# Kernel tuning notes

Measured on AMD Instinct MI355X. Metric: run time of the kernel, lower is better.

## Reference

```python
import jax, jax.numpy as jnp
import numpy as np

TOP_K = 4
EPS = 1e-6


def setup_inputs() -> dict:
    key = jax.random.key(0)
    k1, k2, k3 = jax.random.split(key, 3)
    B, Q, N, H, W = 4, 200, 32, 256, 256
    pred_masks = jax.random.normal(k1, (B, Q, H, W), dtype=jnp.float32)
    pred_logits = jax.random.normal(k2, (B, Q, 2), dtype=jnp.float32)
    gt_masks = (jax.random.uniform(k3, (B, N, H, W)) < 0.3).astype(jnp.float32)
    return {"pred_masks": pred_masks, "pred_logits": pred_logits, "gt_masks": gt_masks}


def _combined_scores(pred_masks, pred_logits, gt_masks):
    """IoU * class-score, shape [B, Q, N]."""
    pm = jax.nn.sigmoid(pred_masks)                    # [B,Q,H,W]
    cls = jax.nn.softmax(pred_logits, axis=-1)[..., 1]  # [B,Q]
    B, Q = pm.shape[:2]
    N = gt_masks.shape[1]
    pmf = pm.reshape(B, Q, -1)                         # [B,Q,D]
    tmf = gt_masks.reshape(B, N, -1)                   # [B,N,D]
    inter = jnp.einsum('bqd,bnd->bqn', pmf, tmf)
    union = pmf.sum(-1)[:, :, None] + tmf.sum(-1)[:, None, :] - inter
    iou = inter / (union + EPS)
    return iou * cls[:, :, None]


def _greedy_assign(combined):
    """Greedy per-GT top-k with dedup. combined: [Q,N] -> sel indices [N,k], -1 = dropped."""
    Q = combined.shape[0]
    k = min(TOP_K, Q)

    def step(assigned, col):
        _, idx = jax.lax.top_k(col, k)          # [k] query indices for this GT
        taken = assigned[idx]                   # already assigned -> drop
        sel = jnp.where(taken, -1, idx)
        assigned = assigned.at[idx].set(True)
        return assigned, sel

    _, sels = jax.lax.scan(step, jnp.zeros(Q, dtype=bool), combined.T)
    return sels  # [N, k]


def reference(pred_masks, pred_logits, gt_masks):
    combined = _combined_scores(pred_masks, pred_logits, gt_masks)  # [B,Q,N]
    sels = jax.vmap(_greedy_assign)(combined)                       # [B,N,k]
    B, N, k = sels.shape
    src_idx = sels
    tgt_idx = jnp.broadcast_to(jnp.arange(N, dtype=jnp.int32)[None, :, None], sels.shape)
    valid = sels >= 0
    tgt_idx = jnp.where(valid, tgt_idx, -1)
    return src_idx, tgt_idx, valid
```

## Files before the change

### kernel.cpp

```cpp
#include <hip/hip_runtime.h>
#include <math.h>
#include <stdint.h>

#define BB    4
#define QQ    200
#define NGT   32
#define DD    65536
#define TOPK  4
#define EPSF  1e-6f
#define QP    208

#define QT16  13
#define KG    32
#define KSPAN (DD / KG)
#define KQ    (KSPAN / 4)
#define NIT   (KQ / 32)

typedef float  f32x4  __attribute__((ext_vector_type(4)));
typedef __bf16 bf16x8 __attribute__((ext_vector_type(8)));

#define PERM_HI16 0x07060302u
#define PERM_LO16 0x05040100u

__global__ __launch_bounds__(256) void k_pack(const float* __restrict__ gt,
                                              uint32_t* __restrict__ packed,
                                              float* __restrict__ zero_base) {
    int zidx = blockIdx.x * 256 + threadIdx.x;
    if (zidx < BB * NGT * QP + BB * QP) zero_base[zidx] = 0.0f;

    int blk = blockIdx.x;
    int b = blk >> 6;
    int d0 = ((blk & 63) * 256 + threadIdx.x) * 4;
    uint32_t px = 0, py = 0, pz = 0, pw = 0;
    const float* gb = gt + (size_t)b * NGT * DD + d0;
#pragma unroll
    for (int n = 0; n < NGT; ++n) {
        float4 g = *(const float4*)(gb + (size_t)n * DD);
        px |= (g.x > 0.5f ? 1u : 0u) << n;
        py |= (g.y > 0.5f ? 1u : 0u) << n;
        pz |= (g.z > 0.5f ? 1u : 0u) << n;
        pw |= (g.w > 0.5f ? 1u : 0u) << n;
    }
    *(uint4*)(packed + (size_t)b * DD + d0) = make_uint4(px, py, pz, pw);
}

__global__ __launch_bounds__(256) void k_tsum(const uint32_t* __restrict__ packed,
                                              float* __restrict__ tsum) {
    int b = blockIdx.x >> 5;
    int n = blockIdx.x & 31;
    const uint4* pp = (const uint4*)(packed + (size_t)b * DD);
    int cnt = 0;
    for (int i = threadIdx.x; i < DD / 4; i += 256) {
        uint4 w = pp[i];
        cnt += (int)((w.x >> n) & 1u) + (int)((w.y >> n) & 1u) +
               (int)((w.z >> n) & 1u) + (int)((w.w >> n) & 1u);
    }
#pragma unroll
    for (int off = 32; off; off >>= 1) cnt += __shfl_xor(cnt, off);
    __shared__ int red[4];
    if ((threadIdx.x & 63) == 0) red[threadIdx.x >> 6] = cnt;
    __syncthreads();
    if (threadIdx.x == 0)
        tsum[blockIdx.x] = (float)(red[0] + red[1] + red[2] + red[3]);
}

__global__ __launch_bounds__(256) void k_mfma(const float* __restrict__ pm,
                                              const uint32_t* __restrict__ packed,
                                              float* __restrict__ inter,
                                              float* __restrict__ psum) {
    int blk = blockIdx.x;
    int b   = blk / (QT16 * KG);
    int rem = blk % (QT16 * KG);
    int qt  = rem / KG;
    int kg  = rem % KG;
    int tid = threadIdx.x, lane = tid & 63, wave = tid >> 6;
    int m = lane & 15, quad = lane >> 4;

    int qg_m = qt * 16 + m;
    int qrow = qg_m < QQ ? qg_m : QQ - 1;

    const float*    ap = pm + ((size_t)b * QQ + qrow) * DD
                            + (size_t)kg * KSPAN + wave * KQ + quad * 8;
    const uint32_t* bp = packed + (size_t)b * DD
                                + (size_t)kg * KSPAN + wave * KQ + quad * 8;

    f32x4 cH0 = {0.f,0.f,0.f,0.f}, cL0 = {0.f,0.f,0.f,0.f};
    f32x4 cH1 = {0.f,0.f,0.f,0.f}, cL1 = {0.f,0.f,0.f,0.f};
    float ps = 0.f;

#pragma unroll 2
    for (int it = 0; it < NIT; ++it) {
        float4 a0 = *(const float4*)(ap + it * 32);
        float4 a1 = *(const float4*)(ap + it * 32 + 4);
        uint4  w0 = *(const uint4*)(bp + it * 32);
        uint4  w1 = *(const uint4*)(bp + it * 32 + 4);

        float xs[8] = {a0.x, a0.y, a0.z, a0.w, a1.x, a1.y, a1.z, a1.w};
        uint32_t hu[8], mu[8], lu[8];
#pragma unroll
        for (int i = 0; i < 8; ++i) {
            float x  = xs[i];
            float sg = __builtin_amdgcn_rcpf(1.0f + __expf(-x));
            ps += sg;
            uint32_t u0 = __float_as_uint(sg);
            float hi = __uint_as_float(u0 & 0xFFFF0000u);
            float r1 = sg - hi;
            uint32_t u1 = __float_as_uint(r1);
            float mi = __uint_as_float(u1 & 0xFFFF0000u);
            float r2 = r1 - mi;
            hu[i] = u0; mu[i] = u1; lu[i] = __float_as_uint(r2);
        }
        union { uint4 u; bf16x8 v; } ah, am, al;
        ah.u = make_uint4(__builtin_amdgcn_perm(hu[1], hu[0], PERM_HI16),
                          __builtin_amdgcn_perm(hu[3], hu[2], PERM_HI16),
                          __builtin_amdgcn_perm(hu[5], hu[4], PERM_HI16),
                          __builtin_amdgcn_perm(hu[7], hu[6], PERM_HI16));
        am.u = make_uint4(__builtin_amdgcn_perm(mu[1], mu[0], PERM_HI16),
                          __builtin_amdgcn_perm(mu[3], mu[2], PERM_HI16),
                          __builtin_amdgcn_perm(mu[5], mu[4], PERM_HI16),
                          __builtin_amdgcn_perm(mu[7], mu[6], PERM_HI16));
        al.u = make_uint4(__builtin_amdgcn_perm(lu[1], lu[0], PERM_HI16),
                          __builtin_amdgcn_perm(lu[3], lu[2], PERM_HI16),
                          __builtin_amdgcn_perm(lu[5], lu[4], PERM_HI16),
                          __builtin_amdgcn_perm(lu[7], lu[6], PERM_HI16));

        uint32_t wj[8] = {w0.x, w0.y, w0.z, w0.w, w1.x, w1.y, w1.z, w1.w};
        uint32_t ob[8];
#pragma unroll
        for (int j = 0; j < 8; ++j) {
            uint32_t t = wj[j] >> m;
            ob[j] = (t & 0x10001u) * 0x3F80u;
        }
        union { uint4 u; bf16x8 v; } b0, b1;
        b0.u = make_uint4(__builtin_amdgcn_perm(ob[1], ob[0], PERM_LO16),
                          __builtin_amdgcn_perm(ob[3], ob[2], PERM_LO16),
                          __builtin_amdgcn_perm(ob[5], ob[4], PERM_LO16),
                          __builtin_amdgcn_perm(ob[7], ob[6], PERM_LO16));
        b1.u = make_uint4(__builtin_amdgcn_perm(ob[1], ob[0], PERM_HI16),
                          __builtin_amdgcn_perm(ob[3], ob[2], PERM_HI16),
                          __builtin_amdgcn_perm(ob[5], ob[4], PERM_HI16),
                          __builtin_amdgcn_perm(ob[7], ob[6], PERM_HI16));

        cH0 = __builtin_amdgcn_mfma_f32_16x16x32_bf16(ah.v, b0.v, cH0, 0, 0, 0);
        cL0 = __builtin_amdgcn_mfma_f32_16x16x32_bf16(am.v, b0.v, cL0, 0, 0, 0);
        cL0 = __builtin_amdgcn_mfma_f32_16x16x32_bf16(al.v, b0.v, cL0, 0, 0, 0);
        cH1 = __builtin_amdgcn_mfma_f32_16x16x32_bf16(ah.v, b1.v, cH1, 0, 0, 0);
        cL1 = __builtin_amdgcn_mfma_f32_16x16x32_bf16(am.v, b1.v, cL1, 0, 0, 0);
        cL1 = __builtin_amdgcn_mfma_f32_16x16x32_bf16(al.v, b1.v, cL1, 0, 0, 0);
    }

    ps += __shfl_xor(ps, 16);
    ps += __shfl_xor(ps, 32);
    if (lane < 16) {
        int qg = qt * 16 + m;
        if (qg < QQ) atomicAdd(&psum[b * QP + qg], ps);
    }

    __shared__ float cred[3 * 64 * 9];
    float c8[8];
#pragma unroll
    for (int r = 0; r < 4; ++r) {
        c8[r]     = cH0[r] + cL0[r];
        c8[4 + r] = cH1[r] + cL1[r];
    }
    __syncthreads();
    if (wave > 0) {
        float* dst = cred + ((wave - 1) * 64 + lane) * 9;
#pragma unroll
        for (int r = 0; r < 8; ++r) dst[r] = c8[r];
    }
    __syncthreads();
    if (wave == 0) {
#pragma unroll
        for (int wv = 0; wv < 3; ++wv) {
            const float* sp = cred + (wv * 64 + lane) * 9;
#pragma unroll
            for (int r = 0; r < 8; ++r) c8[r] += sp[r];
        }
#pragma unroll
        for (int r = 0; r < 4; ++r) {
            int qg = qt * 16 + quad * 4 + r;
            if (qg < QQ) {
                atomicAdd(&inter[(b * NGT + m) * QP + qg],      c8[r]);
                atomicAdd(&inter[(b * NGT + 16 + m) * QP + qg], c8[4 + r]);
            }
        }
    }
}

__global__ __launch_bounds__(256) void k_match(const float* __restrict__ inter,
                                               const float* __restrict__ psum,
                                               const float* __restrict__ tsum,
                                               const float* __restrict__ logits,
                                               int* __restrict__ out) {
    int b = blockIdx.x;
    int tid = threadIdx.x, lane = tid & 63, wave = tid >> 6;
    __shared__ int sidx[NGT][TOPK];

    for (int nn = 0; nn < 8; ++nn) {
        int n  = wave * 8 + nn;
        int bn = b * NGT + n;
        float tsn = tsum[bn];
        float v[4];
#pragma unroll
        for (int s = 0; s < 4; ++s) {
            int q = lane + 64 * s;
            if (q < QQ) {
                float iv = inter[(size_t)bn * QP + q];
                float un = psum[b * QP + q] + tsn - iv;
                float l0 = logits[(b * QQ + q) * 2];
                float l1 = logits[(b * QQ + q) * 2 + 1];
                float cl = 1.0f / (1.0f + expf(l0 - l1));
                v[s] = iv / (un + EPSF) * cl;
            } else {
                v[s] = -INFINITY;
            }
        }
        for (int k = 0; k < TOPK; ++k) {
            float bv = -INFINITY;
            int   bi = 0x7fffffff;
#pragma unroll
            for (int s = 0; s < 4; ++s)
                if (v[s] > bv) { bv = v[s]; bi = lane + 64 * s; }
#pragma unroll
            for (int off = 32; off; off >>= 1) {
                float ov = __shfl_xor(bv, off);
                int   oi = __shfl_xor(bi, off);
                if (ov > bv || (ov == bv && oi < bi)) { bv = ov; bi = oi; }
            }
            if (lane == (bi & 63)) v[bi >> 6] = -INFINITY;
            if (lane == 0) sidx[n][k] = bi;
        }
    }
    __syncthreads();

    if (wave == 0) {
        int* src = out;
        int* tgt = out + BB * NGT * TOPK;
        int* val = out + 2 * BB * NGT * TOPK;
        int asg = 0;
        for (int n = 0; n < NGT; ++n) {
            int ids[4] = {sidx[n][0], sidx[n][1], sidx[n][2], sidx[n][3]};
            int newasg = asg;
#pragma unroll
            for (int k = 0; k < TOPK; ++k) {
                int idx = ids[k];
                int owner = idx & 63, slot = idx >> 6;
                int oasg = __shfl(asg, owner);
                int taken = (oasg >> slot) & 1;
                if (lane == owner) newasg |= (1 << slot);
                if (lane == 0) {
                    int o = (b * NGT + n) * TOPK + k;
                    src[o] = taken ? -1 : idx;
                    tgt[o] = taken ? -1 : n;
                    val[o] = taken ? 0 : 1;
                }
            }
            asg = newasg;
        }
    }
}

extern "C" void kernel_launch(void* const* d_in, const int* in_sizes, int n_in,
                              void* d_out, int out_size, void* d_ws, size_t ws_size,
                              hipStream_t stream) {
    const float* pred_masks  = (const float*)d_in[0];
    const float* pred_logits = (const float*)d_in[1];
    const float* gt_masks    = (const float*)d_in[2];

    uint8_t* ws = (uint8_t*)d_ws;
    uint32_t* packed = (uint32_t*)ws;
    float* tsum  = (float*)(ws + (size_t)BB * DD * 4);
    float* inter = tsum + BB * NGT;
    float* psum  = inter + BB * NGT * QP;

    k_pack <<<BB * (DD / 1024), 256, 0, stream>>>(gt_masks, packed, inter);
    k_tsum <<<BB * NGT,         256, 0, stream>>>(packed, tsum);
    k_mfma <<<BB * QT16 * KG,   256, 0, stream>>>(pred_masks, packed, inter, psum);
    k_match<<<BB,               256, 0, stream>>>(inter, psum, tsum, pred_logits, (int*)d_out);
}
```

Before: 364.7 us.

## Stage pred-mask tiles through LDS with double-buffered async global_load_lds

The MFMA kernel now loads the 16-row pred_masks tile into a double-buffered LDS array using global_load_lds with XOR swizzling, prefetching the next 256-wide chunk while computing the current one. Each wave reads its fragment from LDS instead of issuing strided per-lane global loads, and the reduction scratch reuses the same LDS buffer. The aim is coalesced, overlapped loading of the dominant 200×65536 float stream. In exchange it adds a full vmcnt drain and a barrier per chunk, plus 32KB of LDS per block, which may lower occupancy.

```diff
diff --git a/kernel.cpp b/kernel.cpp
--- a/kernel.cpp
+++ b/kernel.cpp
@@ -13,14 +13,22 @@
 #define QT16  13
 #define KG    32
 #define KSPAN (DD / KG)
-#define KQ    (KSPAN / 4)
-#define NIT   (KQ / 32)
+#define BK    256
+#define NCH   (KSPAN / BK)
 
 typedef float  f32x4  __attribute__((ext_vector_type(4)));
 typedef __bf16 bf16x8 __attribute__((ext_vector_type(8)));
 
 #define PERM_HI16 0x07060302u
 #define PERM_LO16 0x05040100u
+
+#define RAW_BARRIER() asm volatile("s_barrier" ::: "memory")
+#define VM_DRAIN()    asm volatile("s_waitcnt vmcnt(0)" ::: "memory")
+
+#define GLOAD_LDS16(gptr, lptr)                                                  \
+    __builtin_amdgcn_global_load_lds(                                            \
+        (const __attribute__((address_space(1))) uint32_t*)(gptr),               \
+        (__attribute__((address_space(3))) uint32_t*)(lptr), 16, 0, 0)
 
 __global__ __launch_bounds__(256) void k_pack(const float* __restrict__ gt,
                                               uint32_t* __restrict__ packed,
@@ -76,77 +84,110 @@
     int tid = threadIdx.x, lane = tid & 63, wave = tid >> 6;
     int m = lane & 15, quad = lane >> 4;
 
-    int qg_m = qt * 16 + m;
-    int qrow = qg_m < QQ ? qg_m : QQ - 1;
-
-    const float*    ap = pm + ((size_t)b * QQ + qrow) * DD
-                            + (size_t)kg * KSPAN + wave * KQ + quad * 8;
-    const uint32_t* bp = packed + (size_t)b * DD
-                                + (size_t)kg * KSPAN + wave * KQ + quad * 8;
+    __shared__ float sA[2][16][BK];
+
+    const float*    pmb = pm + (size_t)b * QQ * DD + (size_t)kg * KSPAN;
+    const uint32_t* pkb = packed + (size_t)b * DD + (size_t)kg * KSPAN;
+
+    int row0 = wave * 4;
+    int qrow[4];
+#pragma unroll
+    for (int i = 0; i < 4; ++i) {
+        int qg = qt * 16 + row0 + i;
+        qrow[i] = qg < QQ ? qg : QQ - 1;
+    }
 
     f32x4 cH0 = {0.f,0.f,0.f,0.f}, cL0 = {0.f,0.f,0.f,0.f};
     f32x4 cH1 = {0.f,0.f,0.f,0.f}, cL1 = {0.f,0.f,0.f,0.f};
     float ps = 0.f;
 
-#pragma unroll 2
-    for (int it = 0; it < NIT; ++it) {
-        float4 a0 = *(const float4*)(ap + it * 32);
-        float4 a1 = *(const float4*)(ap + it * 32 + 4);
-        uint4  w0 = *(const uint4*)(bp + it * 32);
-        uint4  w1 = *(const uint4*)(bp + it * 32 + 4);
-
-        float xs[8] = {a0.x, a0.y, a0.z, a0.w, a1.x, a1.y, a1.z, a1.w};
-        uint32_t hu[8], mu[8], lu[8];
-#pragma unroll
-        for (int i = 0; i < 8; ++i) {
-            float x  = xs[i];
-            float sg = __builtin_amdgcn_rcpf(1.0f + __expf(-x));
-            ps += sg;
-            uint32_t u0 = __float_as_uint(sg);
-            float hi = __uint_as_float(u0 & 0xFFFF0000u);
-            float r1 = sg - hi;
-            uint32_t u1 = __float_as_uint(r1);
-            float mi = __uint_as_float(u1 & 0xFFFF0000u);
-            float r2 = r1 - mi;
-            hu[i] = u0; mu[i] = u1; lu[i] = __float_as_uint(r2);
-        }
-        union { uint4 u; bf16x8 v; } ah, am, al;
-        ah.u = make_uint4(__builtin_amdgcn_perm(hu[1], hu[0], PERM_HI16),
-                          __builtin_amdgcn_perm(hu[3], hu[2], PERM_HI16),
-                          __builtin_amdgcn_perm(hu[5], hu[4], PERM_HI16),
-                          __builtin_amdgcn_perm(hu[7], hu[6], PERM_HI16));
-        am.u = make_uint4(__builtin_amdgcn_perm(mu[1], mu[0], PERM_HI16),
-                          __builtin_amdgcn_perm(mu[3], mu[2], PERM_HI16),
-                          __builtin_amdgcn_perm(mu[5], mu[4], PERM_HI16),
-                          __builtin_amdgcn_perm(mu[7], mu[6], PERM_HI16));
-        al.u = make_uint4(__builtin_amdgcn_perm(lu[1], lu[0], PERM_HI16),
-                          __builtin_amdgcn_perm(lu[3], lu[2], PERM_HI16),
-                          __builtin_amdgcn_perm(lu[5], lu[4], PERM_HI16),
-                          __builtin_amdgcn_perm(lu[7], lu[6], PERM_HI16));
-
-        uint32_t wj[8] = {w0.x, w0.y, w0.z, w0.w, w1.x, w1.y, w1.z, w1.w};
-        uint32_t ob[8];
-#pragma unroll
-        for (int j = 0; j < 8; ++j) {
-            uint32_t t = wj[j] >> m;
-            ob[j] = (t & 0x10001u) * 0x3F80u;
-        }
-        union { uint4 u; bf16x8 v; } b0, b1;
-        b0.u = make_uint4(__builtin_amdgcn_perm(ob[1], ob[0], PERM_LO16),
-                          __builtin_amdgcn_perm(ob[3], ob[2], PERM_LO16),
-                          __builtin_amdgcn_perm(ob[5], ob[4], PERM_LO16),
-                          __builtin_amdgcn_perm(ob[7], ob[6], PERM_LO16));
-        b1.u = make_uint4(__builtin_amdgcn_perm(ob[1], ob[0], PERM_HI16),
-                          __builtin_amdgcn_perm(ob[3], ob[2], PERM_HI16),
-                          __builtin_amdgcn_perm(ob[5], ob[4], PERM_HI16),
-                          __builtin_amdgcn_perm(ob[7], ob[6], PERM_HI16));
-
-        cH0 = __builtin_amdgcn_mfma_f32_16x16x32_bf16(ah.v, b0.v, cH0, 0, 0, 0);
-        cL0 = __builtin_amdgcn_mfma_f32_16x16x32_bf16(am.v, b0.v, cL0, 0, 0, 0);
-        cL0 = __builtin_amdgcn_mfma_f32_16x16x32_bf16(al.v, b0.v, cL0, 0, 0, 0);
-        cH1 = __builtin_amdgcn_mfma_f32_16x16x32_bf16(ah.v, b1.v, cH1, 0, 0, 0);
-        cL1 = __builtin_amdgcn_mfma_f32_16x16x32_bf16(am.v, b1.v, cL1, 0, 0, 0);
-        cL1 = __builtin_amdgcn_mfma_f32_16x16x32_bf16(al.v, b1.v, cL1, 0, 0, 0);
+#pragma unroll
+    for (int i = 0; i < 4; ++i) {
+        int r = row0 + i;
+        const float* gsrc = pmb + (size_t)qrow[i] * DD + ((lane ^ (r & 7)) << 2);
+        GLOAD_LDS16(gsrc, &sA[0][r][0]);
+    }
+    VM_DRAIN();
+    RAW_BARRIER();
+
+    for (int c = 0; c < NCH; ++c) {
+        int buf = c & 1;
+        if (c + 1 < NCH) {
+#pragma unroll
+            for (int i = 0; i < 4; ++i) {
+                int r = row0 + i;
+                const float* gsrc = pmb + (size_t)qrow[i] * DD
+                                        + (size_t)(c + 1) * BK + ((lane ^ (r & 7)) << 2);
+                GLOAD_LDS16(gsrc, &sA[buf ^ 1][r][0]);
+            }
+        }
+
+#pragma unroll
+        for (int st = 0; st < 2; ++st) {
+            int k0 = wave * 64 + st * 32 + quad * 8;
+            int c0 = k0 >> 2;
+            float4 a0 = *(const float4*)&sA[buf][m][(c0 ^ (m & 7)) << 2];
+            float4 a1 = *(const float4*)&sA[buf][m][((c0 + 1) ^ (m & 7)) << 2];
+            const uint32_t* bpc = pkb + (size_t)c * BK + k0;
+            uint4 w0 = *(const uint4*)(bpc);
+            uint4 w1 = *(const uint4*)(bpc + 4);
+
+            float xs[8] = {a0.x, a0.y, a0.z, a0.w, a1.x, a1.y, a1.z, a1.w};
+            uint32_t hu[8], mu[8], lu[8];
+#pragma unroll
+            for (int i = 0; i < 8; ++i) {
+                float x  = xs[i];
+                float sg = __builtin_amdgcn_rcpf(1.0f + __expf(-x));
+                ps += sg;
+                uint32_t u0 = __float_as_uint(sg);
+                float hi = __uint_as_float(u0 & 0xFFFF0000u);
+                float r1 = sg - hi;
+                uint32_t u1 = __float_as_uint(r1);
+                float mi = __uint_as_float(u1 & 0xFFFF0000u);
+                float r2 = r1 - mi;
+                hu[i] = u0; mu[i] = u1; lu[i] = __float_as_uint(r2);
+            }
+            union { uint4 u; bf16x8 v; } ah, am, al;
+            ah.u = make_uint4(__builtin_amdgcn_perm(hu[1], hu[0], PERM_HI16),
+                              __builtin_amdgcn_perm(hu[3], hu[2], PERM_HI16),
+                              __builtin_amdgcn_perm(hu[5], hu[4], PERM_HI16),
+                              __builtin_amdgcn_perm(hu[7], hu[6], PERM_HI16));
+            am.u = make_uint4(__builtin_amdgcn_perm(mu[1], mu[0], PERM_HI16),
+                              __builtin_amdgcn_perm(mu[3], mu[2], PERM_HI16),
+                              __builtin_amdgcn_perm(mu[5], mu[4], PERM_HI16),
+                              __builtin_amdgcn_perm(mu[7], mu[6], PERM_HI16));
+            al.u = make_uint4(__builtin_amdgcn_perm(lu[1], lu[0], PERM_HI16),
+                              __builtin_amdgcn_perm(lu[3], lu[2], PERM_HI16),
+                              __builtin_amdgcn_perm(lu[5], lu[4], PERM_HI16),
+                              __builtin_amdgcn_perm(lu[7], lu[6], PERM_HI16));
+
+            uint32_t wj[8] = {w0.x, w0.y, w0.z, w0.w, w1.x, w1.y, w1.z, w1.w};
+            uint32_t ob[8];
+#pragma unroll
+            for (int j = 0; j < 8; ++j) {
+                uint32_t t = wj[j] >> m;
+                ob[j] = (t & 0x10001u) * 0x3F80u;
+            }
+            union { uint4 u; bf16x8 v; } b0, b1;
+            b0.u = make_uint4(__builtin_amdgcn_perm(ob[1], ob[0], PERM_LO16),
+                              __builtin_amdgcn_perm(ob[3], ob[2], PERM_LO16),
+                              __builtin_amdgcn_perm(ob[5], ob[4], PERM_LO16),
+                              __builtin_amdgcn_perm(ob[7], ob[6], PERM_LO16));
+            b1.u = make_uint4(__builtin_amdgcn_perm(ob[1], ob[0], PERM_HI16),
+                              __builtin_amdgcn_perm(ob[3], ob[2], PERM_HI16),
+                              __builtin_amdgcn_perm(ob[5], ob[4], PERM_HI16),
+                              __builtin_amdgcn_perm(ob[7], ob[6], PERM_HI16));
+
+            cH0 = __builtin_amdgcn_mfma_f32_16x16x32_bf16(ah.v, b0.v, cH0, 0, 0, 0);
+            cL0 = __builtin_amdgcn_mfma_f32_16x16x32_bf16(am.v, b0.v, cL0, 0, 0, 0);
+            cL0 = __builtin_amdgcn_mfma_f32_16x16x32_bf16(al.v, b0.v, cL0, 0, 0, 0);
+            cH1 = __builtin_amdgcn_mfma_f32_16x16x32_bf16(ah.v, b1.v, cH1, 0, 0, 0);
+            cL1 = __builtin_amdgcn_mfma_f32_16x16x32_bf16(am.v, b1.v, cL1, 0, 0, 0);
+            cL1 = __builtin_amdgcn_mfma_f32_16x16x32_bf16(al.v, b1.v, cL1, 0, 0, 0);
+        }
+
+        if (c + 1 < NCH) VM_DRAIN();
+        RAW_BARRIER();
     }
 
     ps += __shfl_xor(ps, 16);
@@ -156,7 +197,6 @@
         if (qg < QQ) atomicAdd(&psum[b * QP + qg], ps);
     }
 
-    __shared__ float cred[3 * 64 * 9];
     float c8[8];
 #pragma unroll
     for (int r = 0; r < 4; ++r) {
@@ -164,6 +204,7 @@
         c8[4 + r] = cH1[r] + cL1[r];
     }
     __syncthreads();
+    float* cred = (float*)sA;
     if (wave > 0) {
         float* dst = cred + ((wave - 1) * 64 + lane) * 9;
 #pragma unroll
```

Result: no change. 363.8 us (-0.2%).
